# Kernel optimization log

Measured on AMD Instinct MI355X. Metric: run time of the kernel, lower is better.

The kernel has to match this reference:

```python
import jax, jax.numpy as jnp
import numpy as np

N, F_IN, F_HID, N_HEADS, F_OUT, ALPHA = 4096, 128, 64, 4, 64, 0.2
AVG_DEG = 32.0


def setup_inputs() -> dict:
    key = jax.random.key(0)
    ks = jax.random.split(key, 8)
    x = jax.random.normal(ks[0], (N, F_IN), dtype=jnp.float32)
    # sparse-ish adjacency (avg degree ~32) + self loops so every row has a neighbor
    adj = (jax.random.uniform(ks[1], (N, N)) < (AVG_DEG / N)).astype(jnp.float32)
    adj = jnp.maximum(adj, jnp.eye(N, dtype=jnp.float32))
    s = 1.0 / np.sqrt(F_IN)
    lin_W = jax.random.uniform(ks[2], (F_IN, F_IN), jnp.float32, -s, s)
    lin_b = jax.random.uniform(ks[3], (F_IN,), jnp.float32, -s, s)
    W_heads = jax.random.normal(ks[4], (N_HEADS, F_IN, F_HID), jnp.float32) * 0.1
    a_heads = jax.random.normal(ks[5], (N_HEADS, 2 * F_HID), jnp.float32) * 0.1
    W_end = jax.random.normal(ks[6], (N_HEADS * F_HID, F_OUT), jnp.float32) * 0.1
    a_end = jax.random.normal(ks[7], (2 * F_OUT,), jnp.float32) * 0.1
    return dict(x=x, adj=adj, lin_W=lin_W, lin_b=lin_b,
                W_heads=W_heads, a_heads=a_heads, W_end=W_end, a_end=a_end)


def _gat_layer(h, adj, W, a):
    # standard dense-masked GAT layer (pyGAT style)
    Wh = h @ W                      # [N, F']
    f = W.shape[1]
    src = Wh @ a[:f]                # [N]  a^T contribution of source node
    dst = Wh @ a[f:]                # [N]  contribution of destination node
    e = jax.nn.leaky_relu(src[:, None] + dst[None, :], ALPHA)  # [N, N]
    e = jnp.where(adj > 0, e, -9e15)
    att = jax.nn.softmax(e, axis=1)  # neighbor softmax per row
    return jax.nn.elu(att @ Wh)      # [N, F']


def reference(x, adj, lin_W, lin_b, W_heads, a_heads, W_end, a_end):
    h = x @ lin_W + lin_b            # nn.Linear(input_features, input_features)
    # parallel multi-head attention, then concat along feature dim
    heads = jax.vmap(lambda W, a: _gat_layer(h, adj, W, a))(W_heads, a_heads)  # [H, N, F_HID]
    hcat = jnp.transpose(heads, (1, 0, 2)).reshape(N, N_HEADS * F_HID)         # [N, H*F_HID]
    out = _gat_layer(hcat, adj, W_end, a_end)                                  # [N, F_OUT]
    return jax.nn.softmax(out, axis=1)
```

## Files before the change

kernel.cpp:

```cpp
#include <hip/hip_runtime.h>

#define GN 4096
#define F_IN 128
#define F_HID 64
#define NHEADS 4
#define F_OUT 64
#define ALPHA 0.2f
#define MAX_DEG 128
#define NGEMM 512

#define OFF_WH     0
#define OFF_SRC1   4194304
#define OFF_DST1   4259840
#define OFF_WH2    4325376
#define OFF_SRC2   5373952
#define OFF_DST2   5390336
#define OFF_CNT    5406720
#define OFF_IDX    5423104

__global__ __launch_bounds__(256) void prep_kernel(
        const float* __restrict__ adj, const float* __restrict__ x,
        const float* __restrict__ linW, const float* __restrict__ linb,
        const float* __restrict__ Wheads, const float* __restrict__ aheads,
        float* __restrict__ Wh, float* __restrict__ src1, float* __restrict__ dst1,
        int* __restrict__ cnt, int* __restrict__ idx) {
    __shared__ union {
        struct { int sidx[4][264]; int scnt[4]; } c;
        struct { float xs[8][128]; float hs[8][128]; } g;
    } sm;
    const int tid = threadIdx.x;
    const int wave = tid >> 6, lane = tid & 63;

    if (blockIdx.x >= NGEMM) {
        const int row = blockIdx.x - NGEMM;
        const float4* a4 = (const float4*)(adj + (size_t)row * GN) + wave * 256 + lane * 4;
        float4 v0 = a4[0], v1 = a4[1], v2 = a4[2], v3 = a4[3];
        unsigned msk = 0;
        msk |= (v0.x > 0.0f) ? 1u : 0u;         msk |= (v0.y > 0.0f) ? 2u : 0u;
        msk |= (v0.z > 0.0f) ? 4u : 0u;         msk |= (v0.w > 0.0f) ? 8u : 0u;
        msk |= (v1.x > 0.0f) ? 16u : 0u;        msk |= (v1.y > 0.0f) ? 32u : 0u;
        msk |= (v1.z > 0.0f) ? 64u : 0u;        msk |= (v1.w > 0.0f) ? 128u : 0u;
        msk |= (v2.x > 0.0f) ? 256u : 0u;       msk |= (v2.y > 0.0f) ? 512u : 0u;
        msk |= (v2.z > 0.0f) ? 1024u : 0u;      msk |= (v2.w > 0.0f) ? 2048u : 0u;
        msk |= (v3.x > 0.0f) ? 4096u : 0u;      msk |= (v3.y > 0.0f) ? 8192u : 0u;
        msk |= (v3.z > 0.0f) ? 16384u : 0u;     msk |= (v3.w > 0.0f) ? 32768u : 0u;
        const int c = __popc(msk);
        int inc = c;
        #pragma unroll
        for (int o = 1; o < 64; o <<= 1) {
            int n = __shfl_up(inc, o, 64);
            if (lane >= o) inc += n;
        }
        int p = inc - c;
        const int colbase = wave * 1024 + lane * 16;
        #pragma unroll
        for (int b = 0; b < 16; ++b) {
            if (msk & (1u << b)) {
                if (p < 264) sm.c.sidx[wave][p] = colbase + b;
                ++p;
            }
        }
        if (lane == 63) sm.c.scnt[wave] = inc;
        __syncthreads();
        int base = 0;
        #pragma unroll
        for (int w = 0; w < 3; ++w) base += (w < wave) ? sm.c.scnt[w] : 0;
        const int wcount = sm.c.scnt[wave];
        const int total = sm.c.scnt[0] + sm.c.scnt[1] + sm.c.scnt[2] + sm.c.scnt[3];
        const int cc = (total > MAX_DEG) ? MAX_DEG : total;
        int* outp = idx + (size_t)row * MAX_DEG;
        for (int t = lane; t < wcount; t += 64) {
            int pos = base + t;
            if (pos < MAX_DEG) outp[pos] = sm.c.sidx[wave][t];
        }
        if (tid < 4) {
            int pad = ((cc + 3) & ~3) - cc;
            if (tid < pad) outp[cc + tid] = 0;
            if (tid == 0) cnt[row] = cc;
        }
        return;
    }

    const int i0 = blockIdx.x * 8;
    #pragma unroll
    for (int t = 0; t < 4; ++t) {
        int e = t * 256 + tid;
        sm.g.xs[e >> 7][e & 127] = x[(size_t)i0 * 128 + e];
    }
    __syncthreads();
    {
        const int k = tid & 127;
        const int n0 = tid >> 7;
        float bk = linb[k];
        float a0 = bk, a1 = bk, a2 = bk, a3 = bk;
        for (int j = 0; j < 128; ++j) {
            float w = linW[j * 128 + k];
            a0 += sm.g.xs[n0][j] * w;
            a1 += sm.g.xs[n0 + 2][j] * w;
            a2 += sm.g.xs[n0 + 4][j] * w;
            a3 += sm.g.xs[n0 + 6][j] * w;
        }
        sm.g.hs[n0][k] = a0; sm.g.hs[n0 + 2][k] = a1;
        sm.g.hs[n0 + 4][k] = a2; sm.g.hs[n0 + 6][k] = a3;
    }
    __syncthreads();
    {
        const int hd = tid >> 6, f = tid & 63;
        float acc[8] = {0, 0, 0, 0, 0, 0, 0, 0};
        const float* Wp = Wheads + (size_t)hd * F_IN * F_HID + f;
        for (int j = 0; j < 128; ++j) {
            float w = Wp[j * 64];
            #pragma unroll
            for (int n = 0; n < 8; ++n) acc[n] += sm.g.hs[n][j] * w;
        }
        const float as = aheads[hd * 128 + f];
        const float ad = aheads[hd * 128 + 64 + f];
        #pragma unroll
        for (int n = 0; n < 8; ++n) {
            Wh[(size_t)(i0 + n) * 256 + hd * 64 + f] = acc[n];
            float sv = acc[n] * as, dv = acc[n] * ad;
            #pragma unroll
            for (int o = 32; o > 0; o >>= 1) {
                sv += __shfl_xor(sv, o, 64);
                dv += __shfl_xor(dv, o, 64);
            }
            if (f == 0) { src1[(i0 + n) * 4 + hd] = sv; dst1[(i0 + n) * 4 + hd] = dv; }
        }
    }
}

__global__ __launch_bounds__(256) void attn_mid_kernel(
        const float* __restrict__ Wh, const float* __restrict__ src1,
        const float* __restrict__ dst1, const float* __restrict__ Wend,
        const float* __restrict__ aend, float* __restrict__ Wh2,
        float* __restrict__ src2, float* __restrict__ dst2,
        const int* __restrict__ cnt, const int* __restrict__ idx) {
    __shared__ float ps[4][528];
    __shared__ float hcat[4][256];
    const int wave = threadIdx.x >> 6;
    const int lane = threadIdx.x & 63;
    const int row  = blockIdx.x * 4 + wave;
    const int deg  = cnt[row];
    const int* nb  = idx + (size_t)row * MAX_DEG;
    const int nchunk = (deg + 63) >> 6;

    const float4 s4 = ((const float4*)src1)[row];
    float4 ev[2];
    float4 m4 = make_float4(-1e30f, -1e30f, -1e30f, -1e30f);
    for (int c = 0; c < nchunk; ++c) {
        int t = c * 64 + lane;
        float4 e = make_float4(-1e30f, -1e30f, -1e30f, -1e30f);
        if (t < deg) {
            int j = nb[t];
            float4 d = ((const float4*)dst1)[j];
            e.x = s4.x + d.x; e.x = (e.x > 0.0f) ? e.x : ALPHA * e.x;
            e.y = s4.y + d.y; e.y = (e.y > 0.0f) ? e.y : ALPHA * e.y;
            e.z = s4.z + d.z; e.z = (e.z > 0.0f) ? e.z : ALPHA * e.z;
            e.w = s4.w + d.w; e.w = (e.w > 0.0f) ? e.w : ALPHA * e.w;
        }
        ev[c] = e;
        m4.x = fmaxf(m4.x, e.x); m4.y = fmaxf(m4.y, e.y);
        m4.z = fmaxf(m4.z, e.z); m4.w = fmaxf(m4.w, e.w);
    }
    #pragma unroll
    for (int o = 32; o > 0; o >>= 1) {
        m4.x = fmaxf(m4.x, __shfl_xor(m4.x, o, 64));
        m4.y = fmaxf(m4.y, __shfl_xor(m4.y, o, 64));
        m4.z = fmaxf(m4.z, __shfl_xor(m4.z, o, 64));
        m4.w = fmaxf(m4.w, __shfl_xor(m4.w, o, 64));
    }
    float4 l4 = make_float4(0.f, 0.f, 0.f, 0.f);
    for (int c = 0; c < nchunk; ++c) {
        ev[c].x = expf(ev[c].x - m4.x); l4.x += ev[c].x;
        ev[c].y = expf(ev[c].y - m4.y); l4.y += ev[c].y;
        ev[c].z = expf(ev[c].z - m4.z); l4.z += ev[c].z;
        ev[c].w = expf(ev[c].w - m4.w); l4.w += ev[c].w;
    }
    #pragma unroll
    for (int o = 32; o > 0; o >>= 1) {
        l4.x += __shfl_xor(l4.x, o, 64);
        l4.y += __shfl_xor(l4.y, o, 64);
        l4.z += __shfl_xor(l4.z, o, 64);
        l4.w += __shfl_xor(l4.w, o, 64);
    }
    const float4 inv = make_float4(1.f / l4.x, 1.f / l4.y, 1.f / l4.z, 1.f / l4.w);
    for (int c = 0; c < nchunk; ++c) {
        int t = c * 64 + lane;
        float4 p = make_float4(ev[c].x * inv.x, ev[c].y * inv.y,
                               ev[c].z * inv.z, ev[c].w * inv.w);
        ((float4*)&ps[wave][0])[t] = p;
    }

    const int hl = lane >> 4;
    const float4* Wh4 = (const float4*)Wh;
    float4 acc = make_float4(0.f, 0.f, 0.f, 0.f);
    const int deg4 = (deg + 3) & ~3;
    for (int t = 0; t < deg4; t += 4) {
        int4 jj = *(const int4*)(nb + t);
        float4 w0 = Wh4[(size_t)jj.x * 64 + lane];
        float4 w1 = Wh4[(size_t)jj.y * 64 + lane];
        float4 w2 = Wh4[(size_t)jj.z * 64 + lane];
        float4 w3 = Wh4[(size_t)jj.w * 64 + lane];
        const float* pp = &ps[wave][t * 4 + hl];
        float p0 = pp[0], p1 = pp[4], p2 = pp[8], p3 = pp[12];
        acc.x += p0 * w0.x + p1 * w1.x + p2 * w2.x + p3 * w3.x;
        acc.y += p0 * w0.y + p1 * w1.y + p2 * w2.y + p3 * w3.y;
        acc.z += p0 * w0.z + p1 * w1.z + p2 * w2.z + p3 * w3.z;
        acc.w += p0 * w0.w + p1 * w1.w + p2 * w2.w + p3 * w3.w;
    }
    acc.x = (acc.x > 0.0f) ? acc.x : expm1f(acc.x);
    acc.y = (acc.y > 0.0f) ? acc.y : expm1f(acc.y);
    acc.z = (acc.z > 0.0f) ? acc.z : expm1f(acc.z);
    acc.w = (acc.w > 0.0f) ? acc.w : expm1f(acc.w);
    ((float4*)hcat[wave])[lane] = acc;

    float a0 = 0.f, a1 = 0.f, a2 = 0.f, a3 = 0.f;
    const float* Wp = Wend + lane;
    #pragma unroll 4
    for (int j = 0; j < 256; j += 4) {
        a0 += hcat[wave][j    ] * Wp[(j    ) * 64];
        a1 += hcat[wave][j + 1] * Wp[(j + 1) * 64];
        a2 += hcat[wave][j + 2] * Wp[(j + 2) * 64];
        a3 += hcat[wave][j + 3] * Wp[(j + 3) * 64];
    }
    float aa = (a0 + a1) + (a2 + a3);
    Wh2[(size_t)row * 64 + lane] = aa;
    float s0 = aa * aend[lane], d0 = aa * aend[64 + lane];
    #pragma unroll
    for (int o = 32; o > 0; o >>= 1) {
        s0 += __shfl_xor(s0, o, 64); d0 += __shfl_xor(d0, o, 64);
    }
    if (lane == 0) { src2[row] = s0; dst2[row] = d0; }
}

__global__ __launch_bounds__(256) void attn2_kernel(
        const float* __restrict__ Wh2, const float* __restrict__ src,
        const float* __restrict__ dst, const int* __restrict__ cnt,
        const int* __restrict__ idx, float* __restrict__ out) {
    const int wave = threadIdx.x >> 6;
    const int lane = threadIdx.x & 63;
    const int row  = blockIdx.x * 4 + wave;
    const int deg = cnt[row];
    const int* nb = idx + (size_t)row * MAX_DEG;
    const float s_i = src[row];

    float e[2];
    #pragma unroll
    for (int c = 0; c < 2; ++c) {
        int t = c * 64 + lane;
        float ev = -1e30f;
        if (t < deg) {
            int j = nb[t];
            ev = s_i + dst[j];
            ev = (ev > 0.0f) ? ev : ALPHA * ev;
        }
        e[c] = ev;
    }
    float m = fmaxf(e[0], e[1]);
    #pragma unroll
    for (int o = 32; o > 0; o >>= 1) m = fmaxf(m, __shfl_xor(m, o, 64));
    float l = 0.0f;
    #pragma unroll
    for (int c = 0; c < 2; ++c) { e[c] = expf(e[c] - m); l += e[c]; }
    #pragma unroll
    for (int o = 32; o > 0; o >>= 1) l += __shfl_xor(l, o, 64);

    float accA = 0.0f, accB = 0.0f;
    const float* W2 = Wh2 + lane;
    #pragma unroll
    for (int c = 0; c < 2; ++c) {
        int base = c * 64;
        if (base >= deg) break;
        int nmax = deg - base; if (nmax > 64) nmax = 64;
        int n4 = (nmax + 3) & ~3;
        for (int t = 0; t < n4; t += 4) {
            int4 jj = *(const int4*)(nb + base + t);
            float w0 = W2[(size_t)jj.x * 64];
            float w1 = W2[(size_t)jj.y * 64];
            float w2 = W2[(size_t)jj.z * 64];
            float w3 = W2[(size_t)jj.w * 64];
            float p0 = __shfl(e[c], t, 64),     p1 = __shfl(e[c], t + 1, 64);
            float p2 = __shfl(e[c], t + 2, 64), p3 = __shfl(e[c], t + 3, 64);
            accA += p0 * w0 + p2 * w2;
            accB += p1 * w1 + p3 * w3;
        }
    }
    float v = (accA + accB) / l;
    v = (v > 0.0f) ? v : expm1f(v);

    float mm = v;
    #pragma unroll
    for (int o = 32; o > 0; o >>= 1) mm = fmaxf(mm, __shfl_xor(mm, o, 64));
    float ee = expf(v - mm);
    float ss = ee;
    #pragma unroll
    for (int o = 32; o > 0; o >>= 1) ss += __shfl_xor(ss, o, 64);
    out[(size_t)row * F_OUT + lane] = ee / ss;
}

extern "C" void kernel_launch(void* const* d_in, const int* in_sizes, int n_in,
                              void* d_out, int out_size, void* d_ws, size_t ws_size,
                              hipStream_t stream) {
    const float* x      = (const float*)d_in[0];
    const float* adj    = (const float*)d_in[1];
    const float* lin_W  = (const float*)d_in[2];
    const float* lin_b  = (const float*)d_in[3];
    const float* Wheads = (const float*)d_in[4];
    const float* aheads = (const float*)d_in[5];
    const float* Wend   = (const float*)d_in[6];
    const float* aend   = (const float*)d_in[7];
    float* out = (float*)d_out;

    char* ws = (char*)d_ws;
    float* Wh   = (float*)(ws + OFF_WH);
    float* src1 = (float*)(ws + OFF_SRC1);
    float* dst1 = (float*)(ws + OFF_DST1);
    float* Wh2  = (float*)(ws + OFF_WH2);
    float* src2 = (float*)(ws + OFF_SRC2);
    float* dst2 = (float*)(ws + OFF_DST2);
    int*   cnt  = (int*)(ws + OFF_CNT);
    int*   nidx = (int*)(ws + OFF_IDX);

    prep_kernel<<<NGEMM + GN, 256, 0, stream>>>(adj, x, lin_W, lin_b, Wheads, aheads,
                                                Wh, src1, dst1, cnt, nidx);
    attn_mid_kernel<<<GN / 4, 256, 0, stream>>>(Wh, src1, dst1, Wend, aend,
                                                Wh2, src2, dst2, cnt, nidx);
    attn2_kernel<<<GN / 4, 256, 0, stream>>>(Wh2, src2, dst2, cnt, nidx, out);
}
```

Baseline: 57.94 us.

## Store adjacency as bitmask and rebuild neighbor lists inside attention kernels

The prep kernel now writes a 16-bit mask per thread (a 512-byte bitmask per row) instead of doing a block-wide prefix scan and writing compacted neighbor index lists with counts. Both attention kernels rebuild each row's neighbor list in shared memory from the bitmask, using a wave-level prefix sum and a bit-scan loop. This removes the scan, the shared-memory compaction and a __syncthreads from the adjacency pass, and cuts index traffic through global memory. The cost is repeating the compaction in both attention kernels, with a serial per-lane bit loop. Neighbor lists are capped at 136 entries and the attention code still assumes at most 128 neighbors per row.

```diff
diff --git a/kernel.cpp b/kernel.cpp
--- a/kernel.cpp
+++ b/kernel.cpp
@@ -6,7 +6,6 @@
 #define NHEADS 4
 #define F_OUT 64
 #define ALPHA 0.2f
-#define MAX_DEG 128
 #define NGEMM 512
 
 #define OFF_WH     0
@@ -15,25 +14,20 @@
 #define OFF_WH2    4325376
 #define OFF_SRC2   5373952
 #define OFF_DST2   5390336
-#define OFF_CNT    5406720
-#define OFF_IDX    5423104
+#define OFF_BM     5406720
 
 __global__ __launch_bounds__(256) void prep_kernel(
         const float* __restrict__ adj, const float* __restrict__ x,
         const float* __restrict__ linW, const float* __restrict__ linb,
         const float* __restrict__ Wheads, const float* __restrict__ aheads,
         float* __restrict__ Wh, float* __restrict__ src1, float* __restrict__ dst1,
-        int* __restrict__ cnt, int* __restrict__ idx) {
-    __shared__ union {
-        struct { int sidx[4][264]; int scnt[4]; } c;
-        struct { float xs[8][128]; float hs[8][128]; } g;
-    } sm;
+        unsigned short* __restrict__ bm) {
+    __shared__ struct { float xs[8][128]; float hs[8][128]; } sm;
     const int tid = threadIdx.x;
-    const int wave = tid >> 6, lane = tid & 63;
 
     if (blockIdx.x >= NGEMM) {
         const int row = blockIdx.x - NGEMM;
-        const float4* a4 = (const float4*)(adj + (size_t)row * GN) + wave * 256 + lane * 4;
+        const float4* a4 = (const float4*)(adj + (size_t)row * GN) + tid * 4;
         float4 v0 = a4[0], v1 = a4[1], v2 = a4[2], v3 = a4[3];
         unsigned msk = 0;
         msk |= (v0.x > 0.0f) ? 1u : 0u;         msk |= (v0.y > 0.0f) ? 2u : 0u;
@@ -44,40 +38,7 @@
         msk |= (v2.z > 0.0f) ? 1024u : 0u;      msk |= (v2.w > 0.0f) ? 2048u : 0u;
         msk |= (v3.x > 0.0f) ? 4096u : 0u;      msk |= (v3.y > 0.0f) ? 8192u : 0u;
         msk |= (v3.z > 0.0f) ? 16384u : 0u;     msk |= (v3.w > 0.0f) ? 32768u : 0u;
-        const int c = __popc(msk);
-        int inc = c;
-        #pragma unroll
-        for (int o = 1; o < 64; o <<= 1) {
-            int n = __shfl_up(inc, o, 64);
-            if (lane >= o) inc += n;
-        }
-        int p = inc - c;
-        const int colbase = wave * 1024 + lane * 16;
-        #pragma unroll
-        for (int b = 0; b < 16; ++b) {
-            if (msk & (1u << b)) {
-                if (p < 264) sm.c.sidx[wave][p] = colbase + b;
-                ++p;
-            }
-        }
-        if (lane == 63) sm.c.scnt[wave] = inc;
-        __syncthreads();
-        int base = 0;
-        #pragma unroll
-        for (int w = 0; w < 3; ++w) base += (w < wave) ? sm.c.scnt[w] : 0;
-        const int wcount = sm.c.scnt[wave];
-        const int total = sm.c.scnt[0] + sm.c.scnt[1] + sm.c.scnt[2] + sm.c.scnt[3];
-        const int cc = (total > MAX_DEG) ? MAX_DEG : total;
-        int* outp = idx + (size_t)row * MAX_DEG;
-        for (int t = lane; t < wcount; t += 64) {
-            int pos = base + t;
-            if (pos < MAX_DEG) outp[pos] = sm.c.sidx[wave][t];
-        }
-        if (tid < 4) {
-            int pad = ((cc + 3) & ~3) - cc;
-            if (tid < pad) outp[cc + tid] = 0;
-            if (tid == 0) cnt[row] = cc;
-        }
+        bm[row * 256 + tid] = (unsigned short)msk;
         return;
     }
 
@@ -85,7 +46,7 @@
     #pragma unroll
     for (int t = 0; t < 4; ++t) {
         int e = t * 256 + tid;
-        sm.g.xs[e >> 7][e & 127] = x[(size_t)i0 * 128 + e];
+        sm.xs[e >> 7][e & 127] = x[(size_t)i0 * 128 + e];
     }
     __syncthreads();
     {
@@ -95,13 +56,13 @@
         float a0 = bk, a1 = bk, a2 = bk, a3 = bk;
         for (int j = 0; j < 128; ++j) {
             float w = linW[j * 128 + k];
-            a0 += sm.g.xs[n0][j] * w;
-            a1 += sm.g.xs[n0 + 2][j] * w;
-            a2 += sm.g.xs[n0 + 4][j] * w;
-            a3 += sm.g.xs[n0 + 6][j] * w;
-        }
-        sm.g.hs[n0][k] = a0; sm.g.hs[n0 + 2][k] = a1;
-        sm.g.hs[n0 + 4][k] = a2; sm.g.hs[n0 + 6][k] = a3;
+            a0 += sm.xs[n0][j] * w;
+            a1 += sm.xs[n0 + 2][j] * w;
+            a2 += sm.xs[n0 + 4][j] * w;
+            a3 += sm.xs[n0 + 6][j] * w;
+        }
+        sm.hs[n0][k] = a0; sm.hs[n0 + 2][k] = a1;
+        sm.hs[n0 + 4][k] = a2; sm.hs[n0 + 6][k] = a3;
     }
     __syncthreads();
     {
@@ -111,7 +72,7 @@
         for (int j = 0; j < 128; ++j) {
             float w = Wp[j * 64];
             #pragma unroll
-            for (int n = 0; n < 8; ++n) acc[n] += sm.g.hs[n][j] * w;
+            for (int n = 0; n < 8; ++n) acc[n] += sm.hs[n][j] * w;
         }
         const float as = aheads[hd * 128 + f];
         const float ad = aheads[hd * 128 + 64 + f];
@@ -129,19 +90,46 @@
     }
 }
 
+__device__ __forceinline__ int build_row_nbrs(const unsigned short* __restrict__ bm,
+                                              int row, int lane, int* sidx) {
+    unsigned long long bits =
+        ((const unsigned long long*)(bm + (size_t)row * 256))[lane];
+    int c = __popcll(bits);
+    int inc = c;
+    #pragma unroll
+    for (int o = 1; o < 64; o <<= 1) {
+        int n = __shfl_up(inc, o, 64);
+        if (lane >= o) inc += n;
+    }
+    int p = inc - c;
+    const int deg = __shfl(inc, 63, 64);
+    const int col0 = lane * 64;
+    while (bits) {
+        int k = __ffsll((long long)bits) - 1;
+        if (p < 136) sidx[p] = col0 + k;
+        ++p;
+        bits &= bits - 1;
+    }
+    const int deg4 = (deg + 3) & ~3;
+    if (lane < deg4 - deg) sidx[deg + lane] = 0;
+    return deg;
+}
+
 __global__ __launch_bounds__(256) void attn_mid_kernel(
         const float* __restrict__ Wh, const float* __restrict__ src1,
         const float* __restrict__ dst1, const float* __restrict__ Wend,
         const float* __restrict__ aend, float* __restrict__ Wh2,
         float* __restrict__ src2, float* __restrict__ dst2,
-        const int* __restrict__ cnt, const int* __restrict__ idx) {
+        const unsigned short* __restrict__ bm) {
     __shared__ float ps[4][528];
     __shared__ float hcat[4][256];
+    __shared__ int   sidx[4][136];
     const int wave = threadIdx.x >> 6;
     const int lane = threadIdx.x & 63;
     const int row  = blockIdx.x * 4 + wave;
-    const int deg  = cnt[row];
-    const int* nb  = idx + (size_t)row * MAX_DEG;
+
+    const int deg = build_row_nbrs(bm, row, lane, sidx[wave]);
+    const int* nb = sidx[wave];
     const int nchunk = (deg + 63) >> 6;
 
     const float4 s4 = ((const float4*)src1)[row];
@@ -235,13 +223,15 @@
 
 __global__ __launch_bounds__(256) void attn2_kernel(
         const float* __restrict__ Wh2, const float* __restrict__ src,
-        const float* __restrict__ dst, const int* __restrict__ cnt,
-        const int* __restrict__ idx, float* __restrict__ out) {
+        const float* __restrict__ dst, const unsigned short* __restrict__ bm,
+        float* __restrict__ out) {
+    __shared__ int sidx[4][136];
     const int wave = threadIdx.x >> 6;
     const int lane = threadIdx.x & 63;
     const int row  = blockIdx.x * 4 + wave;
-    const int deg = cnt[row];
-    const int* nb = idx + (size_t)row * MAX_DEG;
+
+    const int deg = build_row_nbrs(bm, row, lane, sidx[wave]);
+    const int* nb = sidx[wave];
     const float s_i = src[row];
 
     float e[2];
@@ -318,12 +308,11 @@
     float* Wh2  = (float*)(ws + OFF_WH2);
     float* src2 = (float*)(ws + OFF_SRC2);
     float* dst2 = (float*)(ws + OFF_DST2);
-    int*   cnt  = (int*)(ws + OFF_CNT);
-    int*   nidx = (int*)(ws + OFF_IDX);
+    unsigned short* bm = (unsigned short*)(ws + OFF_BM);
 
     prep_kernel<<<NGEMM + GN, 256, 0, stream>>>(adj, x, lin_W, lin_b, Wheads, aheads,
-                                                Wh, src1, dst1, cnt, nidx);
+                                                Wh, src1, dst1, bm);
     attn_mid_kernel<<<GN / 4, 256, 0, stream>>>(Wh, src1, dst1, Wend, aend,
-                                                Wh2, src2, dst2, cnt, nidx);
-    attn2_kernel<<<GN / 4, 256, 0, stream>>>(Wh2, src2, dst2, cnt, nidx, out);
-}
+                                                Wh2, src2, dst2, bm);
+    attn2_kernel<<<GN / 4, 256, 0, stream>>>(Wh2, src2, dst2, bm, out);
+}
```

New measurement: 56.26 us. -2.9%, faster.
